# Performance work log

Hardware: AMD Instinct MI355X
Metric: run time of the kernel (lower is better)

The kernel has to match this reference:

```python
import math
import jax, jax.numpy as jnp
import numpy as np

B_, L_, D_, N_, R_ = 4, 1024, 1024, 16, 64  # batch, seq, n_embd(=dim_inner), d_state, dt_rank


def setup_inputs() -> dict:
    key = jax.random.key(0)
    ks = jax.random.split(key, 6)
    s = lambda k, shp: jax.random.normal(k, shp, jnp.float32) * 0.02
    return {
        "x": jax.random.normal(ks[0], (B_, L_, D_), jnp.float32),
        "ln1_w": jnp.ones((D_,), jnp.float32),
        "ln2_w": jnp.ones((D_,), jnp.float32),
        "W_dbc": s(ks[1], (R_ + 2 * N_, D_)),   # x -> [delta_lowrank, B, C]
        "W_dt": s(ks[2], (D_, R_)),              # dt_rank -> dim_inner
        "b_dt": jnp.zeros((D_,), jnp.float32),
        "A_log": jnp.log(jnp.broadcast_to(jnp.arange(1, N_ + 1, dtype=jnp.float32), (D_, N_))),
        "Dp": jnp.ones((D_,), jnp.float32),      # skip-connection D parameter
        "W_fc": s(ks[3], (4 * D_, D_)),
        "W_proj": s(ks[4], (D_, 4 * D_)),
    }


def _layernorm(x, w):
    mu = jnp.mean(x, -1, keepdims=True)
    xc = x - mu
    var = jnp.mean(xc * xc, -1, keepdims=True)
    return xc * jax.lax.rsqrt(var + 1e-5) * w


def _new_gelu(x):
    c = math.sqrt(2.0 / math.pi)
    return 0.5 * x * (1.0 + jnp.tanh(c * (x + 0.044715 * x * x * x)))


def _ssm(x, W_dbc, W_dt, b_dt, A_log, Dp):
    # x: (b, l, d) with d == dim_inner == n_embd
    dbc = jnp.einsum("bld,ed->ble", x, W_dbc)                # (b,l,R+2N)
    delta, Bm, Cm = jnp.split(dbc, [R_, R_ + N_], axis=-1)
    delta = jax.nn.softplus(jnp.einsum("blr,dr->bld", delta, W_dt) + b_dt)  # (b,l,d)
    A = -jnp.exp(A_log)                                       # (d,n)
    dA = jnp.exp(delta[..., None] * A)                        # (b,l,d,n) discretized A
    dBx = (delta * x)[..., None] * Bm[:, :, None, :]          # (b,l,d,n) discretized B*x

    # h_t = dA_t * h_{t-1} + dBx_t  -> parallel first-order linear scan
    def combine(e1, e2):
        a1, b1 = e1
        a2, b2 = e2
        return a2 * a1, a2 * b1 + b2

    _, hs = jax.lax.associative_scan(combine, (dA, dBx), axis=1)
    y = jnp.einsum("bldn,bln->bld", hs, Cm)
    return y + x * Dp


def reference(x, ln1_w, ln2_w, W_dbc, W_dt, b_dt, A_log, Dp, W_fc, W_proj):
    h = jax.nn.softplus(_layernorm(x, ln1_w))
    h = h + _ssm(h, W_dbc, W_dt, b_dt, A_log, Dp)
    m = _layernorm(h, ln2_w)
    m = _new_gelu(jnp.einsum("bld,fd->blf", m, W_fc))
    m = jnp.einsum("blf,df->bld", m, W_proj)
    return h + m
```

## Files before the change

kernel.cpp:

```cpp
#include <hip/hip_runtime.h>
#include <cstdint>
#include <cstddef>

typedef unsigned short u16;
typedef unsigned int u32;
typedef __attribute__((ext_vector_type(8))) short short8;
typedef __attribute__((ext_vector_type(4))) float floatx4;
typedef __attribute__((ext_vector_type(4))) u16 u16x4;

#define DEV static __device__ __forceinline__

DEV u16 f2b(float f){ u32 u = __float_as_uint(f); u32 r = u + 0x7fffu + ((u>>16)&1u); return (u16)(r>>16); }
DEV float softplusf(float z){ return fmaxf(z,0.f) + log1pf(__expf(-fabsf(z))); }
DEV float fast_tanhf(float u){ float e = __expf(2.f*u); return 1.f - 2.f/(e+1.f); }
DEV float geluf(float x){ float u = 0.7978845608028654f*(x + 0.044715f*x*x*x); return 0.5f*x*(1.f+fast_tanhf(u)); }

DEV void async_copy16(const void* gp, void* lp){
  __builtin_amdgcn_global_load_lds((const __attribute__((address_space(1))) u32*)gp,
                                   (__attribute__((address_space(3))) u32*)lp, 16, 0, 0);
}

__global__ __launch_bounds__(256)
void prep_weights(const float* __restrict__ Wdbc, const float* __restrict__ Wdt,
                  const float* __restrict__ Wfc, const float* __restrict__ Wproj,
                  u16* __restrict__ dbc_b, u16* __restrict__ dt_b,
                  u16* __restrict__ fc_b, u16* __restrict__ pj_b)
{
  int i = blockIdx.x*256 + threadIdx.x;
  const float* src; u16* dst; int j;
  if (i < 32768){
    int e = i*4, r = e >> 10;
    if (r >= 96){ u16x4 z = {0,0,0,0}; *(u16x4*)(dbc_b + e) = z; return; }
    src = Wdbc; dst = dbc_b; j = i;
  } else if (i < 49152){ src = Wdt;   dst = dt_b; j = i - 32768; }
  else if (i < 1097728){ src = Wfc;   dst = fc_b; j = i - 49152; }
  else                 { src = Wproj; dst = pj_b; j = i - 1097728; }
  float4 v = ((const float4*)src)[j];
  u16x4 o = { f2b(v.x), f2b(v.y), f2b(v.z), f2b(v.w) };
  *(u16x4*)(dst + j*4) = o;
}

__global__ void dbc_post(const float* __restrict__ p, u16* __restrict__ delta_in,
                         float* __restrict__ BCf){
  int e = blockIdx.x*256 + threadIdx.x;
  int t = e >> 7, c = e & 127;
  float s = 0.f;
  #pragma unroll
  for (int z=0;z<8;z++) s += p[(size_t)z*524288 + e];
  if (c < 64)      delta_in[t*64 + c] = f2b(s);
  else if (c < 96) BCf[t*32 + (c-64)] = s;
}

__global__ void proj_reduce(const float* __restrict__ p, const float* __restrict__ h1f,
                            float* __restrict__ out){
  int i = blockIdx.x*256 + threadIdx.x;
  float4 a = ((const float4*)p)[i];
  float4 b = ((const float4*)(p + (size_t) 4194304))[i];
  float4 c = ((const float4*)(p + (size_t) 8388608))[i];
  float4 d = ((const float4*)(p + (size_t)12582912))[i];
  float4 r = ((const float4*)h1f)[i];
  float4 o = make_float4(a.x+b.x+c.x+d.x+r.x, a.y+b.y+c.y+d.y+r.y,
                         a.z+b.z+c.z+d.z+r.z, a.w+b.w+c.w+d.w+r.w);
  ((float4*)out)[i] = o;
}

__global__ __launch_bounds__(256)
void ln1_kernel(const float* __restrict__ x, const float* __restrict__ w,
                float* __restrict__ h0f, u16* __restrict__ h0b)
{
  int row = blockIdx.x, tid = threadIdx.x;
  const float4* xr = (const float4*)(x + (size_t)row*1024);
  float4 v = xr[tid];
  float s1 = v.x+v.y+v.z+v.w;
  float s2 = v.x*v.x+v.y*v.y+v.z*v.z+v.w*v.w;
  #pragma unroll
  for (int m=1;m<64;m<<=1){ s1 += __shfl_xor(s1,m); s2 += __shfl_xor(s2,m); }
  __shared__ float red[8];
  int wv = tid>>6;
  if ((tid&63)==0){ red[wv]=s1; red[4+wv]=s2; }
  __syncthreads();
  s1 = red[0]+red[1]+red[2]+red[3];
  s2 = red[4]+red[5]+red[6]+red[7];
  float mu  = s1*(1.f/1024.f);
  float var = s2*(1.f/1024.f) - mu*mu;
  float rstd = rsqrtf(var + 1e-5f);
  float4 wv4 = ((const float4*)w)[tid];
  float o0 = softplusf((v.x-mu)*rstd*wv4.x);
  float o1 = softplusf((v.y-mu)*rstd*wv4.y);
  float o2 = softplusf((v.z-mu)*rstd*wv4.z);
  float o3 = softplusf((v.w-mu)*rstd*wv4.w);
  ((float4*)(h0f + (size_t)row*1024))[tid] = make_float4(o0,o1,o2,o3);
  u16x4 ob = { f2b(o0), f2b(o1), f2b(o2), f2b(o3) };
  *(u16x4*)(h0b + (size_t)row*1024 + tid*4) = ob;
}

__global__ __launch_bounds__(256)
void ln2_kernel(const float* __restrict__ x, const float* __restrict__ w,
                u16* __restrict__ outb)
{
  int row = blockIdx.x, tid = threadIdx.x;
  const float4* xr = (const float4*)(x + (size_t)row*1024);
  float4 v = xr[tid];
  float s1 = v.x+v.y+v.z+v.w;
  float s2 = v.x*v.x+v.y*v.y+v.z*v.z+v.w*v.w;
  #pragma unroll
  for (int m=1;m<64;m<<=1){ s1 += __shfl_xor(s1,m); s2 += __shfl_xor(s2,m); }
  __shared__ float red[8];
  int wv = tid>>6;
  if ((tid&63)==0){ red[wv]=s1; red[4+wv]=s2; }
  __syncthreads();
  s1 = red[0]+red[1]+red[2]+red[3];
  s2 = red[4]+red[5]+red[6]+red[7];
  float mu  = s1*(1.f/1024.f);
  float var = s2*(1.f/1024.f) - mu*mu;
  float rstd = rsqrtf(var + 1e-5f);
  float4 wv4 = ((const float4*)w)[tid];
  u16x4 ob = { f2b((v.x-mu)*rstd*wv4.x), f2b((v.y-mu)*rstd*wv4.y),
               f2b((v.z-mu)*rstd*wv4.z), f2b((v.w-mu)*rstd*wv4.w) };
  *(u16x4*)(outb + (size_t)row*1024 + tid*4) = ob;
}

template<int EPI, int SWZ>
__global__ __launch_bounds__(256)
void gemm_bt(const u16* __restrict__ A, int lda,
             const u16* __restrict__ B, int ldb, int K,
             float* __restrict__ outF, u16* __restrict__ outB, int ldo,
             const float* __restrict__ bias, size_t zstr)
{
  __shared__ u16 sA[128*32];
  __shared__ u16 sB[128*32];
  const int tid = threadIdx.x;
  int m_blk, n_blk, zb;
  if (SWZ == 0){ n_blk = blockIdx.x; m_blk = blockIdx.y; zb = blockIdx.z; }
  else if (SWZ == 1){
    int b = blockIdx.x, xcd = b & 7, local = b >> 3;
    m_blk = (xcd>>2)*16 + (local & 15);
    n_blk = (xcd&3)*8 + (local >> 4);
    zb = 0;
  } else {
    int b = blockIdx.x, xcd = b & 7, local = b >> 3;
    m_blk = (xcd>>1)*8 + (local & 7);
    n_blk = local >> 3;
    zb = xcd & 1;
  }
  const int m0 = m_blk*128, n0 = n_blk*128;
  const int kstart = zb * K;
  const int wave = tid>>6, lane = tid&63;
  const int wm = (wave>>1)*64, wn = (wave&1)*64;
  const int lr = lane&15, quad = lane>>4;

  floatx4 acc[4][4];
  #pragma unroll
  for (int i=0;i<4;i++)
    #pragma unroll
    for (int j=0;j<4;j++){ floatx4 z = {0.f,0.f,0.f,0.f}; acc[i][j]=z; }

  const int r0 = tid>>2;
  const int kc8 = (((tid&3) ^ ((tid>>3)&3)))*8;
  const int sswz = ((lr>>1)&3);
  for (int k0=kstart; k0<kstart+K; k0+=32){
    __syncthreads();
    async_copy16(A + (size_t)(m0+r0)*lda    + k0+kc8, &sA[(size_t)tid*8]);
    async_copy16(A + (size_t)(m0+64+r0)*lda + k0+kc8, &sA[(size_t)(tid+256)*8]);
    async_copy16(B + (size_t)(n0+r0)*ldb    + k0+kc8, &sB[(size_t)tid*8]);
    async_copy16(B + (size_t)(n0+64+r0)*ldb + k0+kc8, &sB[(size_t)(tid+256)*8]);
    __syncthreads();
    short8 af[4], bf[4];
    #pragma unroll
    for (int i=0;i<4;i++){
      af[i] = *(const short8*)&sA[(wm+i*16+lr)*32 + (quad^sswz)*8];
      bf[i] = *(const short8*)&sB[(wn+i*16+lr)*32 + (quad^sswz)*8];
    }
    #pragma unroll
    for (int i=0;i<4;i++)
      #pragma unroll
      for (int j=0;j<4;j++)
        acc[i][j] = __builtin_amdgcn_mfma_f32_16x16x32_bf16(af[i], bf[j], acc[i][j], 0,0,0);
  }
  #pragma unroll
  for (int i=0;i<4;i++){
    #pragma unroll
    for (int j=0;j<4;j++){
      #pragma unroll
      for (int r=0;r<4;r++){
        int gr = m0 + wm + i*16 + quad*4 + r;
        int gc = n0 + wn + j*16 + lr;
        float v = acc[i][j][r];
        size_t o = (size_t)gr*ldo + gc;
        if (EPI==1)      outF[o] = softplusf(v + bias[gc]);
        else if (EPI==2) outB[o] = f2b(geluf(v));
        else             outF[zstr*zb + o] = v;
      }
    }
  }
}

template<int EPI, int SWZ>
__global__ __launch_bounds__(512, 2)
void gemm256(const u16* __restrict__ A, int lda,
             const u16* __restrict__ B, int ldb, int K,
             float* __restrict__ outF, u16* __restrict__ outB, int ldo,
             size_t zstr)
{
  __shared__ u16 sA[2][4][4096];
  __shared__ u16 sB[2][4][4096];
  const int tid = threadIdx.x;
  int m_blk, n_blk, zb;
  if (SWZ == 3){
    int b = blockIdx.x, xcd = b & 7, local = b >> 3;
    m_blk = (xcd>>2)*8 + (local & 7);
    n_blk = (xcd&3)*4 + (local >> 3);
    zb = 0;
  } else {
    int b = blockIdx.x, xcd = b & 7, local = b >> 3;
    zb    = xcd >> 1;
    m_blk = (xcd&1)*8 + (local & 7);
    n_blk = local >> 3;
  }
  const int m0 = m_blk*256, n0 = n_blk*256;
  const int kstart = zb*K;
  const int wave = tid>>6, lane = tid&63;
  const int mq = wave>>2, nq = wave&3;
  const int lr = lane&15, quad = lane>>4;
  const int sswz = (lr>>1)&3;

  const int srow = tid>>2;
  const int scol = ((tid&3) ^ ((tid>>3)&3))*8;
  const u16* pa = A + (size_t)(m0 + srow)*lda + scol;
  const u16* pb = B + (size_t)(n0 + srow)*ldb + scol;
  u16* la = (u16*)sA + tid*8;
  u16* lb = (u16*)sB + tid*8;
  const size_t ah128 = (size_t)128*lda;
  const size_t bh128 = (size_t)128*ldb;

  const int a_rd = (mq*64 + lr)*32 + (quad^sswz)*8;
  const int b_rd = ((nq&1)*64 + lr)*32 + (quad^sswz)*8;
  const int bun  = nq>>1;

  floatx4 acc[2][4][4];
  #pragma unroll
  for (int h=0;h<2;h++)
    #pragma unroll
    for (int i=0;i<4;i++)
      #pragma unroll
      for (int j=0;j<4;j++){ floatx4 z={0.f,0.f,0.f,0.f}; acc[h][i][j]=z; }

  short8 af[4], bf[4];

#define STG_A(NB,KS,H,KT) async_copy16(pa + (size_t)(H)*ah128 + (size_t)((KT) + (KS)*32), \
                                       la + (NB)*16384 + ((KS)*2+(H))*4096)
#define STG_B(NB,KS,H,KT) async_copy16(pb + (size_t)(H)*bh128 + (size_t)((KT) + (KS)*32), \
                                       lb + (NB)*16384 + ((KS)*2+(H))*4096)

#define PHASE(CUR, KS, AH, VM, ...)                                           \
  {                                                                           \
    const u16* ca = (const u16*)sA + (CUR)*16384 + ((KS)*2+(AH))*4096;        \
    _Pragma("unroll")                                                         \
    for (int i_=0;i_<4;i_++) af[i_] = *(const short8*)(ca + a_rd + i_*512);   \
    if ((AH)==0){                                                             \
      const u16* cb = (const u16*)sB + (CUR)*16384 + ((KS)*2+bun)*4096;       \
      _Pragma("unroll")                                                       \
      for (int i_=0;i_<4;i_++) bf[i_] = *(const short8*)(cb + b_rd + i_*512); \
    }                                                                         \
    __VA_ARGS__;                                                              \
    __builtin_amdgcn_s_barrier();                                             \
    asm volatile("s_waitcnt lgkmcnt(0)" ::: "memory");                        \
    __builtin_amdgcn_sched_barrier(0);                                        \
    __builtin_amdgcn_s_setprio(1);                                            \
    _Pragma("unroll")                                                         \
    for (int i_=0;i_<4;i_++)                                                  \
      _Pragma("unroll")                                                       \
      for (int j_=0;j_<4;j_++)                                                \
        acc[AH][i_][j_] = __builtin_amdgcn_mfma_f32_16x16x32_bf16(            \
            af[i_], bf[j_], acc[AH][i_][j_], 0,0,0);                          \
    __builtin_amdgcn_s_setprio(0);                                            \
    asm volatile("s_waitcnt vmcnt(" VM ")" ::: "memory");                     \
    __builtin_amdgcn_s_barrier();                                             \
  }

  STG_A(0,0,0,kstart); STG_B(0,0,0,kstart);
  STG_B(0,0,1,kstart); STG_A(0,0,1,kstart);
  STG_B(0,1,0,kstart); STG_B(0,1,1,kstart);
  STG_A(0,1,0,kstart); STG_A(0,1,1,kstart);
  asm volatile("s_waitcnt vmcnt(5)" ::: "memory");
  __builtin_amdgcn_s_barrier();

  const int NT = K >> 6;
  int cur = 0;
  int ktn = kstart + 64;
  for (int t=0; t<NT; ++t, ktn += 64, cur ^= 1){
    const int nb = cur^1;
    const int kt = (t < NT-1) ? ktn : kstart;
    PHASE(cur, 0,0, "6", STG_A(nb,0,0,kt); STG_B(nb,0,0,kt));
    PHASE(cur, 0,1, "5", STG_B(nb,0,1,kt); STG_A(nb,0,1,kt));
    PHASE(cur, 1,0, "6", STG_B(nb,1,0,kt); STG_B(nb,1,1,kt));
    PHASE(cur, 1,1, "5", STG_A(nb,1,0,kt); STG_A(nb,1,1,kt));
  }

#undef PHASE
#undef STG_A
#undef STG_B

  #pragma unroll
  for (int h=0;h<2;h++){
    #pragma unroll
    for (int i=0;i<4;i++){
      #pragma unroll
      for (int j=0;j<4;j++){
        #pragma unroll
        for (int r=0;r<4;r++){
          int gr = m0 + h*128 + mq*64 + i*16 + quad*4 + r;
          int gc = n0 + nq*64 + j*16 + lr;
          float v = acc[h][i][j][r];
          size_t o = (size_t)gr*ldo + gc;
          if (EPI==2) outB[o] = f2b(geluf(v));
          else        outF[zstr*zb + o] = v;
        }
      }
    }
  }
}

__global__ __launch_bounds__(256)
void scan_p1(const float* __restrict__ delta, const float* __restrict__ h0f,
             const float* __restrict__ BCf, const float* __restrict__ A_log,
             float* __restrict__ Pbuf, float* __restrict__ Sbuf)
{
  int blk = blockIdx.x;
  int d = (blk & 3)*256 + threadIdx.x;
  int c = (blk >> 2) & 31;
  int b = blk >> 7;
  float a2[16], h[16], P[16];
  #pragma unroll
  for (int n=0;n<16;n++){ a2[n] = -__expf(A_log[d*16+n]) * 1.44269504f; h[n]=0.f; P[n]=1.f; }
  int t0 = c*32;
  const float* dptr = delta + ((size_t)(b*1024 + t0))*1024 + d;
  const float* xptr = h0f   + ((size_t)(b*1024 + t0))*1024 + d;
  const float* bc   = BCf   + ((size_t)(b*1024 + t0))*32;
  #pragma unroll 4
  for (int t=0;t<32;t++){
    float dlt = dptr[t*1024];
    float xv  = xptr[t*1024];
    float dx = dlt*xv;
    #pragma unroll
    for (int n=0;n<16;n++){
      float dA = exp2f(dlt*a2[n]);
      h[n] = dA*h[n] + dx*bc[t*32+n];
      P[n] *= dA;
    }
  }
  size_t base = ((size_t)((b*32 + c)*16))*1024 + d;
  #pragma unroll
  for (int n=0;n<16;n++){ Pbuf[base + (size_t)n*1024] = P[n]; Sbuf[base + (size_t)n*1024] = h[n]; }
}

__global__ __launch_bounds__(256)
void scan_p2(const float* __restrict__ Pbuf, const float* __restrict__ Sbuf,
             float* __restrict__ Hbuf)
{
  int blk = blockIdx.x;
  int d = (blk & 3)*256 + threadIdx.x;
  int n = (blk >> 2) & 15;
  int b = blk >> 6;
  float H = 0.f;
  for (int c=0;c<32;c++){
    size_t idx = ((size_t)((b*32 + c)*16 + n))*1024 + d;
    float P = Pbuf[idx], S = Sbuf[idx];
    Hbuf[idx] = H;
    H = P*H + S;
  }
}

__global__ __launch_bounds__(256)
void scan_p3(const float* __restrict__ delta, const float* __restrict__ h0f,
             const float* __restrict__ BCf, const float* __restrict__ A_log,
             const float* __restrict__ Hbuf, const float* __restrict__ Dp,
             float* __restrict__ h1f)
{
  int blk = blockIdx.x;
  int d = (blk & 3)*256 + threadIdx.x;
  int c = (blk >> 2) & 31;
  int b = blk >> 7;
  float a2[16], h[16];
  size_t hb = ((size_t)((b*32 + c)*16))*1024 + d;
  #pragma unroll
  for (int n=0;n<16;n++){
    a2[n] = -__expf(A_log[d*16+n]) * 1.44269504f;
    h[n] = Hbuf[hb + (size_t)n*1024];
  }
  float dpv = 1.f + Dp[d];
  int t0 = c*32;
  const float* dptr = delta + ((size_t)(b*1024 + t0))*1024 + d;
  const float* xptr = h0f   + ((size_t)(b*1024 + t0))*1024 + d;
  const float* bc   = BCf   + ((size_t)(b*1024 + t0))*32;
  float* optr = h1f + ((size_t)(b*1024 + t0))*1024 + d;
  #pragma unroll 4
  for (int t=0;t<32;t++){
    float dlt = dptr[t*1024];
    float xv  = xptr[t*1024];
    float dx = dlt*xv;
    float y = 0.f;
    #pragma unroll
    for (int n=0;n<16;n++){
      float dA = exp2f(dlt*a2[n]);
      h[n] = dA*h[n] + dx*bc[t*32+n];
      y += h[n]*bc[t*32+16+n];
    }
    optr[t*1024] = xv*dpv + y;
  }
}

extern "C" void kernel_launch(void* const* d_in, const int* in_sizes, int n_in,
                              void* d_out, int out_size, void* d_ws, size_t ws_size,
                              hipStream_t stream)
{
  const float* x    = (const float*)d_in[0];
  const float* ln1w = (const float*)d_in[1];
  const float* ln2w = (const float*)d_in[2];
  const float* Wdbc = (const float*)d_in[3];
  const float* Wdt  = (const float*)d_in[4];
  const float* bdt  = (const float*)d_in[5];
  const float* Alog = (const float*)d_in[6];
  const float* Dp   = (const float*)d_in[7];
  const float* Wfc  = (const float*)d_in[8];
  const float* Wproj= (const float*)d_in[9];
  float* out = (float*)d_out;

  char* ws = (char*)d_ws;
  size_t off = 0;
  auto carve = [&](size_t bytes)->char*{ char* p = ws + off; off += (bytes + 255) & ~(size_t)255; return p; };
  const size_t T = 4096;
  float* h0f   = (float*)carve(T*1024*4);
  float* h1f   = (float*)carve(T*1024*4);
  float* dlt   = (float*)carve(T*1024*4);
  float* Pbuf  = (float*)carve((size_t)4*32*16*1024*4);
  float* Sbuf  = (float*)carve((size_t)4*32*16*1024*4);
  float* Hbuf  = (float*)carve((size_t)4*32*16*1024*4);
  float* pad_  = (float*)carve((size_t)4*32*16*1024*4);
  float* BCf   = (float*)carve(T*32*4);
  u16*   h0b   = (u16*)  carve(T*1024*2);
  u16*   m0b   = (u16*)  carve(T*1024*2);
  u16*   g_b   = (u16*)  carve(T*4096*2);
  u16*   din_b = (u16*)  carve(T*64*2);
  u16*   Wdbc_b= (u16*)  carve((size_t)128*1024*2);
  u16*   Wdt_b = (u16*)  carve((size_t)1024*64*2);
  u16*   Wfc_b = (u16*)  carve((size_t)4096*1024*2);
  u16*   Wpj_b = (u16*)  carve((size_t)1024*4096*2);
  float* dbc_p  = Hbuf;
  float* proj_p = dlt;
  (void)pad_; (void)ws_size; (void)in_sizes; (void)n_in; (void)out_size;

  prep_weights<<<8384, 256, 0, stream>>>(Wdbc, Wdt, Wfc, Wproj,
                                         Wdbc_b, Wdt_b, Wfc_b, Wpj_b);

  ln1_kernel<<<4096, 256, 0, stream>>>(x, ln1w, h0f, h0b);

  gemm_bt<4,0><<<dim3(1,32,8), 256, 0, stream>>>(h0b, 1024, Wdbc_b, 1024, 128,
                                                 dbc_p, nullptr, 128, nullptr, (size_t)T*128);
  dbc_post<<<2048, 256, 0, stream>>>(dbc_p, din_b, BCf);

  gemm_bt<1,0><<<dim3(8,32), 256, 0, stream>>>(din_b, 64, Wdt_b, 64, 64,
                                               dlt, nullptr, 1024, bdt, 0);

  scan_p1<<<512, 256, 0, stream>>>(dlt, h0f, BCf, Alog, Pbuf, Sbuf);
  scan_p2<<<256, 256, 0, stream>>>(Pbuf, Sbuf, Hbuf);
  scan_p3<<<512, 256, 0, stream>>>(dlt, h0f, BCf, Alog, Hbuf, Dp, h1f);

  ln2_kernel<<<4096, 256, 0, stream>>>(h1f, ln2w, m0b);

  gemm256<2,3><<<256, 512, 0, stream>>>(m0b, 1024, Wfc_b, 1024, 1024,
                                        nullptr, g_b, 4096, 0);

  gemm256<4,4><<<256, 512, 0, stream>>>(g_b, 4096, Wpj_b, 4096, 1024,
                                        proj_p, nullptr, 1024, (size_t)T*1024);
  proj_reduce<<<4096, 256, 0, stream>>>(proj_p, h1f, out);
}
```

Baseline: 333.9 us.

## Double-buffer GEMM register fragments to overlap LDS reads with MFMA

```diff
diff --git a/kernel.cpp b/kernel.cpp
--- a/kernel.cpp
+++ b/kernel.cpp
@@ -245,26 +245,31 @@
       #pragma unroll
       for (int j=0;j<4;j++){ floatx4 z={0.f,0.f,0.f,0.f}; acc[h][i][j]=z; }
 
-  short8 af[4], bf[4];
+  short8 af[2][4], bf[2][4];
 
 #define STG_A(NB,KS,H,KT) async_copy16(pa + (size_t)(H)*ah128 + (size_t)((KT) + (KS)*32), \
                                        la + (NB)*16384 + ((KS)*2+(H))*4096)
 #define STG_B(NB,KS,H,KT) async_copy16(pb + (size_t)(H)*bh128 + (size_t)((KT) + (KS)*32), \
                                        lb + (NB)*16384 + ((KS)*2+(H))*4096)
 
-#define PHASE(CUR, KS, AH, VM, ...)                                           \
+#define PH(MFS, MBS, AH, PRBUF, PRKS, PRAH, PRB, VM, LG, STMTS)               \
   {                                                                           \
-    const u16* ca = (const u16*)sA + (CUR)*16384 + ((KS)*2+(AH))*4096;        \
-    _Pragma("unroll")                                                         \
-    for (int i_=0;i_<4;i_++) af[i_] = *(const short8*)(ca + a_rd + i_*512);   \
-    if ((AH)==0){                                                             \
-      const u16* cb = (const u16*)sB + (CUR)*16384 + ((KS)*2+bun)*4096;       \
+    STMTS;                                                                    \
+    asm volatile("s_waitcnt vmcnt(" VM ")" ::: "memory");                     \
+    __builtin_amdgcn_s_barrier();                                             \
+    {                                                                         \
+      const u16* ca_ = (const u16*)sA + (PRBUF)*16384 + ((PRKS)*2+(PRAH))*4096;\
       _Pragma("unroll")                                                       \
-      for (int i_=0;i_<4;i_++) bf[i_] = *(const short8*)(cb + b_rd + i_*512); \
+      for (int i_=0;i_<4;i_++)                                                \
+        af[(MFS)^1][i_] = *(const short8*)(ca_ + a_rd + i_*512);              \
+      if (PRB){                                                               \
+        const u16* cb_ = (const u16*)sB + (PRBUF)*16384 + ((PRKS)*2+bun)*4096;\
+        _Pragma("unroll")                                                     \
+        for (int i_=0;i_<4;i_++)                                              \
+          bf[(MBS)^1][i_] = *(const short8*)(cb_ + b_rd + i_*512);            \
+      }                                                                       \
     }                                                                         \
-    __VA_ARGS__;                                                              \
-    __builtin_amdgcn_s_barrier();                                             \
-    asm volatile("s_waitcnt lgkmcnt(0)" ::: "memory");                        \
+    asm volatile("s_waitcnt lgkmcnt(" LG ")" ::: "memory");                   \
     __builtin_amdgcn_sched_barrier(0);                                        \
     __builtin_amdgcn_s_setprio(1);                                            \
     _Pragma("unroll")                                                         \
@@ -272,10 +277,8 @@
       _Pragma("unroll")                                                       \
       for (int j_=0;j_<4;j_++)                                                \
         acc[AH][i_][j_] = __builtin_amdgcn_mfma_f32_16x16x32_bf16(            \
-            af[i_], bf[j_], acc[AH][i_][j_], 0,0,0);                          \
+            af[MFS][i_], bf[MBS][j_], acc[AH][i_][j_], 0,0,0);                \
     __builtin_amdgcn_s_setprio(0);                                            \
-    asm volatile("s_waitcnt vmcnt(" VM ")" ::: "memory");                     \
-    __builtin_amdgcn_s_barrier();                                             \
   }
 
   STG_A(0,0,0,kstart); STG_B(0,0,0,kstart);
@@ -284,20 +287,30 @@
   STG_A(0,1,0,kstart); STG_A(0,1,1,kstart);
   asm volatile("s_waitcnt vmcnt(5)" ::: "memory");
   __builtin_amdgcn_s_barrier();
+  {
+    const u16* ca_ = (const u16*)sA;
+    #pragma unroll
+    for (int i_=0;i_<4;i_++) af[0][i_] = *(const short8*)(ca_ + a_rd + i_*512);
+    const u16* cb_ = (const u16*)sB + bun*4096;
+    #pragma unroll
+    for (int i_=0;i_<4;i_++) bf[0][i_] = *(const short8*)(cb_ + b_rd + i_*512);
+  }
 
   const int NT = K >> 6;
-  int cur = 0;
-  int ktn = kstart + 64;
-  for (int t=0; t<NT; ++t, ktn += 64, cur ^= 1){
-    const int nb = cur^1;
-    const int kt = (t < NT-1) ? ktn : kstart;
-    PHASE(cur, 0,0, "6", STG_A(nb,0,0,kt); STG_B(nb,0,0,kt));
-    PHASE(cur, 0,1, "5", STG_B(nb,0,1,kt); STG_A(nb,0,1,kt));
-    PHASE(cur, 1,0, "6", STG_B(nb,1,0,kt); STG_B(nb,1,1,kt));
-    PHASE(cur, 1,1, "5", STG_A(nb,1,0,kt); STG_A(nb,1,1,kt));
-  }
-
-#undef PHASE
+  for (int t=0; t<NT; t+=2){
+    const int ka = kstart + (t+1)*64;
+    const int kb = (t+2 < NT) ? (kstart + (t+2)*64) : kstart;
+    PH(0,0,0, 0,0,1,0, "6","4", STG_A(1,0,0,ka); STG_B(1,0,0,ka));
+    PH(1,0,1, 0,1,0,1, "5","8", STG_B(1,0,1,ka); STG_A(1,0,1,ka));
+    PH(0,1,0, 0,1,1,0, "6","4", STG_B(1,1,0,ka); STG_B(1,1,1,ka));
+    PH(1,1,1, 1,0,0,1, "5","8", STG_A(1,1,0,ka); STG_A(1,1,1,ka));
+    PH(0,0,0, 1,0,1,0, "6","4", STG_A(0,0,0,kb); STG_B(0,0,0,kb));
+    PH(1,0,1, 1,1,0,1, "5","8", STG_B(0,0,1,kb); STG_A(0,0,1,kb));
+    PH(0,1,0, 1,1,1,0, "6","4", STG_B(0,1,0,kb); STG_B(0,1,1,kb));
+    PH(1,1,1, 0,0,0,1, "5","8", STG_A(0,1,0,kb); STG_A(0,1,1,kb));
+  }
+
+#undef PH
 #undef STG_A
 #undef STG_B
 
```

After: 329.6 us. About the same (-1.3%).
